# Optimization experiments

Hardware: AMD Instinct MI355X
Metric: run time of the kernel (lower is better)

The kernel has to match this reference:

```python
import jax, jax.numpy as jnp
import numpy as np
import math

N_GENES_TOTAL = 20000
N_CELLS_TOTAL = 10000
N_LATENT = 64
N_COMP = 32
SCALE_LOWER_BOUND = 1e-5
LOG_2PI = math.log(2.0 * math.pi)


def setup_inputs() -> dict:
    key = jax.random.key(0)
    ks = jax.random.split(key, 16)
    n_cells, n_genes = 512, 4000
    n_cuts, n_frags = 1000000, 1000000
    inp = {}
    inp["local_cellxgene_ix"] = jax.random.randint(ks[0], (n_frags,), 0, n_cells * n_genes)
    inp["cut_coordinates"] = jax.random.uniform(ks[1], (n_cuts,), dtype=jnp.float32)
    inp["latent"] = jax.random.normal(ks[2], (n_cells, N_LATENT), dtype=jnp.float32)
    inp["genes_oi"] = jax.random.randint(ks[3], (n_genes,), 0, N_GENES_TOTAL)
    inp["cells_oi"] = jax.random.randint(ks[4], (n_cells,), 0, N_CELLS_TOTAL)
    inp["cut_local_cellxgene_ix"] = jax.random.randint(ks[5], (n_cuts,), 0, n_cells * n_genes)
    inp["cut_local_gene_ix"] = jax.random.randint(ks[6], (n_cuts,), 0, n_genes)
    inp["n_cells"] = n_cells
    inp["n_genes"] = n_genes
    # Mixture parameters (per total gene)
    loc_init = jnp.linspace(0.0, 1.0, N_COMP + 2)[1:-1]  # (C,)
    inp["loc_w"] = jnp.broadcast_to(jax.scipy.special.logit(loc_init), (N_GENES_TOTAL, N_COMP)).astype(jnp.float32)
    inp["scale_w"] = jnp.full((N_GENES_TOTAL, N_COMP), math.log(1.0 / N_COMP / 5.0), dtype=jnp.float32)
    inp["logit_w"] = (jax.random.normal(ks[7], (N_GENES_TOTAL, N_COMP)) / math.sqrt(N_COMP)).astype(jnp.float32)
    # Decoder sparse embeddings (n_layers=0 -> input dim = n_latent)
    stdv_l = 1.0 / math.sqrt(N_LATENT)
    inp["logit_weight"] = jax.random.uniform(ks[8], (N_GENES_TOTAL, N_LATENT, N_COMP), minval=-stdv_l, maxval=stdv_l, dtype=jnp.float32)
    stdv_r = 1.0 / math.sqrt(N_LATENT) / 100.0
    inp["rho_weight"] = jax.random.uniform(ks[9], (N_GENES_TOTAL, N_LATENT), minval=-stdv_r, maxval=stdv_r, dtype=jnp.float32)
    inp["rho_bias"] = jax.random.uniform(ks[10], (N_GENES_TOTAL,), minval=1e-4, maxval=1e-2, dtype=jnp.float32)
    inp["libsize"] = jax.random.uniform(ks[11], (N_CELLS_TOTAL,), minval=1000.0, maxval=10000.0, dtype=jnp.float32)
    return inp


def reference(local_cellxgene_ix, cut_coordinates, latent, genes_oi, cells_oi,
              cut_local_cellxgene_ix, cut_local_gene_ix, n_cells, n_genes,
              loc_w, scale_w, logit_w, logit_weight, rho_weight, rho_bias, libsize):
    # Decoder (n_layers=0 => nn_output == latent)
    lw = logit_weight[genes_oi]                      # [G, L, C]
    rw = rho_weight[genes_oi]                        # [G, L]
    mixture_delta = jnp.einsum("nl,glc->ngc", latent, lw)   # [N, G, C]
    rho = latent @ rw.T                               # [N, G]

    # Gather per-cut mixture delta
    C = mixture_delta.shape[-1]
    delta = mixture_delta.reshape(-1, C)[cut_local_cellxgene_ix]  # [K, C]

    # Mixture log prob
    loc = jax.nn.sigmoid(loc_w[genes_oi])[cut_local_gene_ix]                 # [K, C]
    scale = SCALE_LOWER_BOUND + jnp.exp(scale_w[genes_oi])[cut_local_gene_ix]  # [K, C]
    logits = logit_w[genes_oi][cut_local_gene_ix] + delta                    # [K, C]
    z = (cut_coordinates[:, None] - loc) / scale
    comp_lp = -0.5 * z * z - jnp.log(scale) - 0.5 * LOG_2PI                  # Normal log_prob
    likelihood_mixture = jax.scipy.special.logsumexp(jax.nn.log_softmax(logits, axis=-1) + comp_lp, axis=-1)  # [K]

    # Fragment count Poisson likelihood
    fragmentexpression = rho_bias[genes_oi][None, :] * jnp.exp(rho) * libsize[cells_oi][:, None]  # [N, G]
    counts = jnp.zeros((n_cells * n_genes,), dtype=jnp.float32).at[local_cellxgene_ix].add(1.0).reshape(n_cells, n_genes)
    likelihood_fragmentcounts = counts * jnp.log(fragmentexpression) - fragmentexpression - jax.lax.lgamma(counts + 1.0)

    elbo = -(likelihood_mixture.sum() + likelihood_fragmentcounts.sum())
    return elbo
```

## Files before the change

### kernel.cpp

```cpp
#include <hip/hip_runtime.h>


#define TPB 256
#define CHUNK 4096
#define MAXG 4096
#define MAXN 1024
#define HALF_LOG_2PI 0.9189385332046727f

typedef short bf16x8 __attribute__((ext_vector_type(8)));
typedef float f32x4 __attribute__((ext_vector_type(4)));

static __device__ __forceinline__ unsigned short f2bf(float f) {
  unsigned u = __float_as_uint(f);
  u += 0x7fffu + ((u >> 16) & 1u);
  return (unsigned short)(u >> 16);
}

static __device__ __forceinline__ float block_reduce(float v) {
  #pragma unroll
  for (int off = 32; off > 0; off >>= 1) v += __shfl_down(v, off, 64);
  __shared__ float wsum[4];
  if ((threadIdx.x & 63) == 0) wsum[threadIdx.x >> 6] = v;
  __syncthreads();
  return (threadIdx.x == 0) ? (wsum[0] + wsum[1] + wsum[2] + wsum[3]) : 0.f;
}

__global__ __launch_bounds__(TPB) void prep_hist_kernel(
    const int* __restrict__ cxg, const int* __restrict__ lix,
    unsigned* __restrict__ cntC, unsigned* __restrict__ cntF,
    const int* __restrict__ genes_oi,
    const float* __restrict__ loc_w, const float* __restrict__ scale_w,
    const float* __restrict__ logit_w, const float* __restrict__ latent,
    float4* __restrict__ gp, unsigned short* __restrict__ latbf,
    int K, int F, unsigned G, unsigned N, int B, int NL) {
  if ((int)blockIdx.x >= B) {
    int idx = ((int)blockIdx.x - B) * TPB + threadIdx.x;
    int ngp = (int)G * 32;
    if (idx < ngp) {
      int g = idx >> 5, c = idx & 31;
      long long gene = genes_oi[g];
      float lv = loc_w[gene * 32 + c];
      float loc = 1.f / (1.f + __expf(-lv));
      float sc = 1e-5f + __expf(scale_w[gene * 32 + c]);
      gp[idx] = make_float4(loc, 1.f / sc, -__logf(sc) - HALF_LOG_2PI, logit_w[gene * 32 + c]);
    } else if (idx - ngp < NL) {
      latbf[idx - ngp] = f2bf(latent[idx - ngp]);
    }
    return;
  }
  __shared__ unsigned hC[MAXG];
  __shared__ unsigned hF[MAXN];
  for (int t = threadIdx.x; t < MAXG; t += TPB) hC[t] = 0;
  for (int t = threadIdx.x; t < MAXN; t += TPB) hF[t] = 0;
  __syncthreads();
  int i0 = blockIdx.x * CHUNK;
  for (int t = threadIdx.x; t < CHUNK; t += TPB) {
    int i = i0 + t;
    if (i < K) { unsigned ix = (unsigned)cxg[i]; atomicAdd(&hC[ix % G], 1u); }
    if (i < F) { unsigned v = (unsigned)lix[i]; atomicAdd(&hF[v / G], 1u); }
  }
  __syncthreads();
  size_t b = blockIdx.x;
  for (unsigned t = threadIdx.x; t < G; t += TPB) cntC[b * G + t] = hC[t];
  for (unsigned t = threadIdx.x; t < N; t += TPB) cntF[b * N + t] = hF[t];
}

__global__ __launch_bounds__(TPB) void colscan_v2(
    unsigned* __restrict__ cntC, unsigned* __restrict__ cntF,
    unsigned* __restrict__ totC, unsigned* __restrict__ totF,
    int B, unsigned G, unsigned N) {
  unsigned wid = blockIdx.x * 4 + (threadIdx.x >> 6);
  int lane = threadIdx.x & 63;
  if (wid >= G + N) return;
  unsigned* col;
  unsigned stride;
  unsigned* tot;
  if (wid < G) { col = cntC + wid; stride = G; tot = totC + wid; }
  else         { col = cntF + (wid - G); stride = N; tot = totF + (wid - G); }
  unsigned base = 0;
  for (int b0 = 0; b0 < B; b0 += 64) {
    int b = b0 + lane;
    unsigned v = (b < B) ? col[(size_t)b * stride] : 0u;
    unsigned inc = v;
    #pragma unroll
    for (int d = 1; d < 64; d <<= 1) {
      unsigned t2 = __shfl_up(inc, d, 64);
      if (lane >= d) inc += t2;
    }
    if (b < B) col[(size_t)b * stride] = inc - v + base;
    base += __shfl(inc, 63, 64);
  }
  if (lane == 0) *tot = base;
}

__global__ __launch_bounds__(TPB) void scan2_v2(
    const unsigned* __restrict__ totC, unsigned* __restrict__ baseC, int SC, unsigned K,
    const unsigned* __restrict__ totF, unsigned* __restrict__ baseF, int SF, unsigned F,
    unsigned* __restrict__ ticket) {
  int lane = threadIdx.x & 63;
  int wv = threadIdx.x >> 6;
  if (wv == 0) {
    unsigned base = 0;
    for (int i0 = 0; i0 < SC; i0 += 64) {
      int i = i0 + lane;
      unsigned v = (i < SC) ? totC[i] : 0u;
      unsigned inc = v;
      #pragma unroll
      for (int d = 1; d < 64; d <<= 1) {
        unsigned t = __shfl_up(inc, d, 64);
        if (lane >= d) inc += t;
      }
      if (i < SC) baseC[i] = inc - v + base;
      base += __shfl(inc, 63, 64);
    }
    if (lane == 0) baseC[SC] = K;
  } else if (wv == 1) {
    unsigned base = 0;
    for (int i0 = 0; i0 < SF; i0 += 64) {
      int i = i0 + lane;
      unsigned v = (i < SF) ? totF[i] : 0u;
      unsigned inc = v;
      #pragma unroll
      for (int d = 1; d < 64; d <<= 1) {
        unsigned t = __shfl_up(inc, d, 64);
        if (lane >= d) inc += t;
      }
      if (i < SF) baseF[i] = inc - v + base;
      base += __shfl(inc, 63, 64);
    }
    if (lane == 0) baseF[SF] = F;
  } else if (threadIdx.x == 128) {
    *ticket = 0u;
  }
}

__global__ __launch_bounds__(TPB) void sort_pass3(
    const int* __restrict__ cxg, const int* __restrict__ lix,
    const float* __restrict__ xc, const int* __restrict__ gix,
    const unsigned* __restrict__ cntC, const unsigned* __restrict__ cntF,
    const unsigned* __restrict__ baseC, const unsigned* __restrict__ baseF,
    float2* __restrict__ pl, unsigned* __restrict__ fpl,
    int K, int F, unsigned G, unsigned N) {
  __shared__ unsigned cC[MAXG];
  __shared__ unsigned cF[MAXN];
  for (int t = threadIdx.x; t < MAXG; t += TPB) cC[t] = 0;
  for (int t = threadIdx.x; t < MAXN; t += TPB) cF[t] = 0;
  __syncthreads();
  int i0 = blockIdx.x * CHUNK;
  size_t b = blockIdx.x;
  for (int t = threadIdx.x; t < CHUNK; t += TPB) {
    int i = i0 + t;
    if (i < K) {
      unsigned ix = (unsigned)cxg[i];
      unsigned g = ix % G, n = ix / G;
      unsigned r = atomicAdd(&cC[g], 1u);
      unsigned pos = baseC[g] + cntC[b * G + g] + r;
      pl[pos] = make_float2(xc[i], __uint_as_float((n << 16) | (unsigned)gix[i]));
    }
    if (i < F) {
      unsigned v = (unsigned)lix[i];
      unsigned n = v / G, g = v - n * G;
      unsigned r = atomicAdd(&cF[n], 1u);
      fpl[baseF[n] + cntF[b * N + n] + r] = (n << 16) | g;
    }
  }
}

__global__ __launch_bounds__(TPB) void cuts_v6(
    const float2* __restrict__ pl, const unsigned short* __restrict__ latbf,
    const int* __restrict__ genes_oi, const float* __restrict__ logit_weight,
    const float4* __restrict__ gp, const unsigned* __restrict__ baseC,
    float* __restrict__ partials, unsigned G) {
  const int g = blockIdx.x;
  const int lane = threadIdx.x & 63;
  const int wv = threadIdx.x >> 6;
  const int quad = lane >> 4;
  const int r16 = lane & 15;

  const float* Wb = logit_weight + (size_t)genes_oi[g] * 2048;
  bf16x8 B0a, B1a, B0b, B1b;
  #pragma unroll
  for (int j = 0; j < 8; j++) {
    int l0 = quad * 8 + j;
    B0a[j] = (short)f2bf(Wb[l0 * 32 + r16]);
    B1a[j] = (short)f2bf(Wb[(l0 + 32) * 32 + r16]);
    B0b[j] = (short)f2bf(Wb[l0 * 32 + r16 + 16]);
    B1b[j] = (short)f2bf(Wb[(l0 + 32) * 32 + r16 + 16]);
  }

  const unsigned start = baseC[g], end = baseC[g + 1];
  const unsigned ntiles = (end - start + 15) >> 4;
  float lm = 0.f;

  for (unsigned t = wv; t < ntiles; t += 4) {
    unsigned kk0 = start + t * 16;
    unsigned idx = kk0 + r16;
    float2 p = pl[idx < end ? idx : start];
    unsigned u = __float_as_uint(p.y);
    const unsigned short* lb = latbf + (size_t)(u >> 16) * 64;
    bf16x8 A0 = *(const bf16x8*)(lb + quad * 8);
    bf16x8 A1 = *(const bf16x8*)(lb + 32 + quad * 8);

    f32x4 acc0 = {0.f, 0.f, 0.f, 0.f};
    f32x4 acc1 = {0.f, 0.f, 0.f, 0.f};
    acc0 = __builtin_amdgcn_mfma_f32_16x16x32_bf16(A0, B0a, acc0, 0, 0, 0);
    acc0 = __builtin_amdgcn_mfma_f32_16x16x32_bf16(A1, B1a, acc0, 0, 0, 0);
    acc1 = __builtin_amdgcn_mfma_f32_16x16x32_bf16(A0, B0b, acc1, 0, 0, 0);
    acc1 = __builtin_amdgcn_mfma_f32_16x16x32_bf16(A1, B1b, acc1, 0, 0, 0);

    #pragma unroll
    for (int r = 0; r < 4; r++) {
      int cut = quad * 4 + r;
      float xr = __shfl(p.x, cut, 64);
      unsigned ur = (unsigned)__shfl((int)u, cut, 64);
      unsigned gi = ur & 0xffffu;
      float4 q0 = gp[(size_t)gi * 32 + r16];
      float4 q1 = gp[(size_t)gi * 32 + r16 + 16];
      float t0 = q0.w + acc0[r], t1 = q1.w + acc1[r];
      float z0 = (xr - q0.x) * q0.y, z1 = (xr - q1.x) * q1.y;
      float u0 = t0 + fmaf(-0.5f * z0, z0, q0.z);
      float u1 = t1 + fmaf(-0.5f * z1, z1, q1.z);
      float e1 = __expf(u0) + __expf(u1);
      float e2 = __expf(t0) + __expf(t1);
      #pragma unroll
      for (int d = 1; d < 16; d <<= 1) {
        e1 += __shfl_xor(e1, d, 64);
        e2 += __shfl_xor(e2, d, 64);
      }
      if (r16 == 0 && (kk0 + (unsigned)cut) < end) lm += __logf(e1) - __logf(e2);
    }
  }
  float bs = block_reduce(lm);
  if (threadIdx.x == 0) partials[blockIdx.x] = bs;
}

__global__ __launch_bounds__(TPB) void pois_v5(
    const unsigned* __restrict__ fpl, const unsigned* __restrict__ baseF,
    const float* __restrict__ latent, const int* __restrict__ genes_oi,
    const int* __restrict__ cells_oi,
    const float* __restrict__ rho_weight, const float* __restrict__ rho_bias,
    const float* __restrict__ libsize,
    float* __restrict__ p1, int n1,
    float* __restrict__ p2, unsigned* __restrict__ ticket,
    float* __restrict__ out, int N, int G) {
  int n0 = blockIdx.x * 2;
  const int PB = gridDim.x;
  __shared__ unsigned cnt[2 * MAXG];
  for (int t = threadIdx.x; t < 2 * MAXG; t += TPB) cnt[t] = 0;
  __shared__ __align__(16) float lat[128];
  for (int t = threadIdx.x; t < 128; t += TPB) {
    int j = t >> 6, l = t & 63;
    lat[t] = (n0 + j < N) ? latent[(size_t)(n0 + j) * 64 + l] : 0.f;
  }
  __syncthreads();
  int nhi = min(n0 + 2, N);
  unsigned s0 = baseF[n0], e0 = baseF[nhi];
  for (unsigned i = s0 + threadIdx.x; i < e0; i += TPB) {
    unsigned v = fpl[i];
    unsigned j = (v >> 16) - (unsigned)n0, g = v & 0xffffu;
    atomicAdd(&cnt[j * MAXG + g], 1u);
  }
  __syncthreads();
  float lib0 = (n0 < N) ? libsize[cells_oi[n0]] : 0.f;
  float lib1 = (n0 + 1 < N) ? libsize[cells_oi[n0 + 1]] : 0.f;
  float sum = 0.f;
  for (int g = threadIdx.x; g < G; g += TPB) {
    long long gene = genes_oi[g];
    const float4* rw = (const float4*)(rho_weight + gene * 64);
    float r0 = 0.f, r1 = 0.f;
    #pragma unroll
    for (int i = 0; i < 16; i++) {
      float4 wv = rw[i];
      float4 l0 = *(const float4*)(&lat[i * 4]);
      float4 l1 = *(const float4*)(&lat[64 + i * 4]);
      r0 = fmaf(wv.x, l0.x, r0); r0 = fmaf(wv.y, l0.y, r0);
      r0 = fmaf(wv.z, l0.z, r0); r0 = fmaf(wv.w, l0.w, r0);
      r1 = fmaf(wv.x, l1.x, r1); r1 = fmaf(wv.y, l1.y, r1);
      r1 = fmaf(wv.z, l1.z, r1); r1 = fmaf(wv.w, l1.w, r1);
    }
    float rb = rho_bias[gene];
    if (n0 < N) {
      float fe = rb * __expf(r0) * lib0;
      unsigned c = cnt[g];
      float term = -fe;
      if (c) {
        float lf = 0.f;
        for (unsigned q2 = 2; q2 <= c; q2++) lf += __logf((float)q2);
        term += (float)c * __logf(fe) - lf;
      }
      sum += term;
    }
    if (n0 + 1 < N) {
      float fe = rb * __expf(r1) * lib1;
      unsigned c = cnt[MAXG + g];
      float term = -fe;
      if (c) {
        float lf = 0.f;
        for (unsigned q2 = 2; q2 <= c; q2++) lf += __logf((float)q2);
        term += (float)c * __logf(fe) - lf;
      }
      sum += term;
    }
  }
  float bs = block_reduce(sum);
  __shared__ unsigned slast;
  if (threadIdx.x == 0) {
    p2[blockIdx.x] = bs;
    __threadfence();
    slast = atomicAdd(ticket, 1u);
  }
  __syncthreads();
  if (slast == (unsigned)(PB - 1)) {
    __threadfence();
    float s = 0.f;
    for (int i = threadIdx.x; i < n1; i += TPB) s += p1[i];
    for (int i = threadIdx.x; i < PB; i += TPB) s += p2[i];
    float tot = block_reduce(s);
    if (threadIdx.x == 0) out[0] = -tot;
  }
}

extern "C" void kernel_launch(void* const* d_in, const int* in_sizes, int n_in,
                              void* d_out, int out_size, void* d_ws, size_t ws_size,
                              hipStream_t stream) {
  const int*   lix          = (const int*)d_in[0];
  const float* xc           = (const float*)d_in[1];
  const float* latent       = (const float*)d_in[2];
  const int*   genes_oi     = (const int*)d_in[3];
  const int*   cells_oi     = (const int*)d_in[4];
  const int*   cxg          = (const int*)d_in[5];
  const int*   gix          = (const int*)d_in[6];
  const float* loc_w        = (const float*)d_in[9];
  const float* scale_w      = (const float*)d_in[10];
  const float* logit_w      = (const float*)d_in[11];
  const float* logit_weight = (const float*)d_in[12];
  const float* rho_weight   = (const float*)d_in[13];
  const float* rho_bias     = (const float*)d_in[14];
  const float* libsize      = (const float*)d_in[15];
  float* out = (float*)d_out;

  const int F = in_sizes[0];
  const int K = in_sizes[1];
  const int N = in_sizes[2] / 64;
  const int G = in_sizes[3];
  const int NL = N * 64;

  const int M = (K > F) ? K : F;
  const int B = (M + CHUNK - 1) / CHUNK;
  const int PB = (N + 1) / 2;
  const int GPB = (G * 32 + NL + TPB - 1) / TPB;

  size_t off = 0;
  auto alloc = [&](size_t bytes) {
    size_t o = off;
    off = (off + bytes + 255) & ~(size_t)255;
    return o;
  };
  size_t cntC_off  = alloc((size_t)B * G * 4);
  size_t cntF_off  = alloc((size_t)B * N * 4);
  size_t totC_off  = alloc((size_t)G * 4);
  size_t totF_off  = alloc((size_t)N * 4);
  size_t baseC_off = alloc((size_t)(G + 1) * 4);
  size_t baseF_off = alloc((size_t)(N + 1) * 4);
  size_t pl_off    = alloc((size_t)K * 8);
  size_t fpl_off   = alloc((size_t)F * 4);
  size_t gp_off    = alloc((size_t)G * 32 * 16);
  size_t lb_off    = alloc((size_t)NL * 2);
  size_t p1_off    = alloc((size_t)G * 4);
  size_t p2_off    = alloc((size_t)PB * 4);
  size_t tk_off    = alloc(4);
  (void)ws_size;

  char* ws = (char*)d_ws;
  unsigned* cntC  = (unsigned*)(ws + cntC_off);
  unsigned* cntF  = (unsigned*)(ws + cntF_off);
  unsigned* totC  = (unsigned*)(ws + totC_off);
  unsigned* totF  = (unsigned*)(ws + totF_off);
  unsigned* baseC = (unsigned*)(ws + baseC_off);
  unsigned* baseF = (unsigned*)(ws + baseF_off);
  float2*   pl    = (float2*)(ws + pl_off);
  unsigned* fpl   = (unsigned*)(ws + fpl_off);
  float4*   gp    = (float4*)(ws + gp_off);
  unsigned short* latbf = (unsigned short*)(ws + lb_off);
  float*    p1    = (float*)(ws + p1_off);
  float*    p2    = (float*)(ws + p2_off);
  unsigned* ticket = (unsigned*)(ws + tk_off);

  prep_hist_kernel<<<B + GPB, TPB, 0, stream>>>(
      cxg, lix, cntC, cntF, genes_oi, loc_w, scale_w, logit_w, latent,
      gp, latbf, K, F, (unsigned)G, (unsigned)N, B, NL);
  colscan_v2<<<(G + N + 3) / 4, TPB, 0, stream>>>(
      cntC, cntF, totC, totF, B, (unsigned)G, (unsigned)N);
  scan2_v2<<<1, TPB, 0, stream>>>(totC, baseC, G, (unsigned)K,
                                  totF, baseF, N, (unsigned)F, ticket);
  sort_pass3<<<B, TPB, 0, stream>>>(cxg, lix, xc, gix, cntC, cntF, baseC, baseF,
                                    pl, fpl, K, F, (unsigned)G, (unsigned)N);
  cuts_v6<<<G, TPB, 0, stream>>>(pl, latbf, genes_oi, logit_weight, gp, baseC, p1, (unsigned)G);
  pois_v5<<<PB, TPB, 0, stream>>>(fpl, baseF, latent, genes_oi, cells_oi,
                                  rho_weight, rho_bias, libsize,
                                  p1, G, p2, ticket, out, N, G);
}
```

Baseline: 447.8 us.

## Bucket fragments by gene, fuse cuts and Poisson kernels, merge scans

Fragments are now bucketed by gene instead of by cell, so the Poisson term is computed per group of 4 genes across all cells. The mixture/cuts work and the Poisson work become one heterogeneous kernel launch with a single last-block reduction. The second-level scan is folded into the column-scan kernel through a last-block ticket. Together these remove two kernel launches and let the cuts and Poisson blocks overlap on the device. The cost is a larger gene-indexed fragment histogram (G columns instead of N) and extra work on the per-column scan and histogram stages.

New measurement: 723.7 us. 1.62x slower.

```diff
diff --git a/kernel.cpp b/kernel.cpp
--- a/kernel.cpp
+++ b/kernel.cpp
@@ -5,6 +5,7 @@
 #define CHUNK 4096
 #define MAXG 4096
 #define MAXN 1024
+#define GPG 4
 #define HALF_LOG_2PI 0.9189385332046727f
 
 typedef short bf16x8 __attribute__((ext_vector_type(8)));
@@ -32,8 +33,10 @@
     const float* __restrict__ loc_w, const float* __restrict__ scale_w,
     const float* __restrict__ logit_w, const float* __restrict__ latent,
     float4* __restrict__ gp, unsigned short* __restrict__ latbf,
-    int K, int F, unsigned G, unsigned N, int B, int NL) {
+    unsigned* __restrict__ ticket2,
+    int K, int F, unsigned G, int B, int NL) {
   if ((int)blockIdx.x >= B) {
+    if ((int)blockIdx.x == B && threadIdx.x == 0) *ticket2 = 0u;
     int idx = ((int)blockIdx.x - B) * TPB + threadIdx.x;
     int ngp = (int)G * 32;
     if (idx < ngp) {
@@ -49,88 +52,92 @@
     return;
   }
   __shared__ unsigned hC[MAXG];
-  __shared__ unsigned hF[MAXN];
-  for (int t = threadIdx.x; t < MAXG; t += TPB) hC[t] = 0;
-  for (int t = threadIdx.x; t < MAXN; t += TPB) hF[t] = 0;
+  __shared__ unsigned hF[MAXG];
+  for (int t = threadIdx.x; t < MAXG; t += TPB) { hC[t] = 0; hF[t] = 0; }
   __syncthreads();
   int i0 = blockIdx.x * CHUNK;
   for (int t = threadIdx.x; t < CHUNK; t += TPB) {
     int i = i0 + t;
     if (i < K) { unsigned ix = (unsigned)cxg[i]; atomicAdd(&hC[ix % G], 1u); }
-    if (i < F) { unsigned v = (unsigned)lix[i]; atomicAdd(&hF[v / G], 1u); }
+    if (i < F) { unsigned v = (unsigned)lix[i]; atomicAdd(&hF[v % G], 1u); }
   }
   __syncthreads();
   size_t b = blockIdx.x;
-  for (unsigned t = threadIdx.x; t < G; t += TPB) cntC[b * G + t] = hC[t];
-  for (unsigned t = threadIdx.x; t < N; t += TPB) cntF[b * N + t] = hF[t];
-}
-
-__global__ __launch_bounds__(TPB) void colscan_v2(
+  for (unsigned t = threadIdx.x; t < G; t += TPB) {
+    cntC[b * G + t] = hC[t];
+    cntF[b * G + t] = hF[t];
+  }
+}
+
+__global__ __launch_bounds__(TPB) void colscan_v3(
     unsigned* __restrict__ cntC, unsigned* __restrict__ cntF,
     unsigned* __restrict__ totC, unsigned* __restrict__ totF,
-    int B, unsigned G, unsigned N) {
+    unsigned* __restrict__ baseC, unsigned* __restrict__ baseF,
+    int B, unsigned G, unsigned K, unsigned F,
+    unsigned* __restrict__ ticket2, unsigned* __restrict__ ticket4, int NBLK) {
   unsigned wid = blockIdx.x * 4 + (threadIdx.x >> 6);
   int lane = threadIdx.x & 63;
-  if (wid >= G + N) return;
-  unsigned* col;
-  unsigned stride;
-  unsigned* tot;
-  if (wid < G) { col = cntC + wid; stride = G; tot = totC + wid; }
-  else         { col = cntF + (wid - G); stride = N; tot = totF + (wid - G); }
-  unsigned base = 0;
-  for (int b0 = 0; b0 < B; b0 += 64) {
-    int b = b0 + lane;
-    unsigned v = (b < B) ? col[(size_t)b * stride] : 0u;
-    unsigned inc = v;
-    #pragma unroll
-    for (int d = 1; d < 64; d <<= 1) {
-      unsigned t2 = __shfl_up(inc, d, 64);
-      if (lane >= d) inc += t2;
-    }
-    if (b < B) col[(size_t)b * stride] = inc - v + base;
-    base += __shfl(inc, 63, 64);
-  }
-  if (lane == 0) *tot = base;
-}
-
-__global__ __launch_bounds__(TPB) void scan2_v2(
-    const unsigned* __restrict__ totC, unsigned* __restrict__ baseC, int SC, unsigned K,
-    const unsigned* __restrict__ totF, unsigned* __restrict__ baseF, int SF, unsigned F,
-    unsigned* __restrict__ ticket) {
-  int lane = threadIdx.x & 63;
-  int wv = threadIdx.x >> 6;
-  if (wv == 0) {
+  if (wid < 2 * G) {
+    unsigned* col = (wid < G) ? (cntC + wid) : (cntF + (wid - G));
+    unsigned* tot = (wid < G) ? (totC + wid) : (totF + (wid - G));
     unsigned base = 0;
-    for (int i0 = 0; i0 < SC; i0 += 64) {
-      int i = i0 + lane;
-      unsigned v = (i < SC) ? totC[i] : 0u;
+    for (int b0 = 0; b0 < B; b0 += 64) {
+      int b = b0 + lane;
+      unsigned v = (b < B) ? col[(size_t)b * G] : 0u;
       unsigned inc = v;
       #pragma unroll
       for (int d = 1; d < 64; d <<= 1) {
-        unsigned t = __shfl_up(inc, d, 64);
-        if (lane >= d) inc += t;
-      }
-      if (i < SC) baseC[i] = inc - v + base;
+        unsigned t2 = __shfl_up(inc, d, 64);
+        if (lane >= d) inc += t2;
+      }
+      if (b < B) col[(size_t)b * G] = inc - v + base;
       base += __shfl(inc, 63, 64);
     }
-    if (lane == 0) baseC[SC] = K;
-  } else if (wv == 1) {
-    unsigned base = 0;
-    for (int i0 = 0; i0 < SF; i0 += 64) {
-      int i = i0 + lane;
-      unsigned v = (i < SF) ? totF[i] : 0u;
-      unsigned inc = v;
-      #pragma unroll
-      for (int d = 1; d < 64; d <<= 1) {
-        unsigned t = __shfl_up(inc, d, 64);
-        if (lane >= d) inc += t;
-      }
-      if (i < SF) baseF[i] = inc - v + base;
-      base += __shfl(inc, 63, 64);
-    }
-    if (lane == 0) baseF[SF] = F;
-  } else if (threadIdx.x == 128) {
-    *ticket = 0u;
+    if (lane == 0) *tot = base;
+  }
+  __syncthreads();
+  __shared__ unsigned sl;
+  if (threadIdx.x == 0) {
+    __threadfence();
+    sl = atomicAdd(ticket2, 1u);
+  }
+  __syncthreads();
+  if (sl == (unsigned)(NBLK - 1)) {
+    __threadfence();
+    int wv = threadIdx.x >> 6;
+    if (wv == 0) {
+      unsigned base = 0;
+      for (int i0 = 0; i0 < (int)G; i0 += 64) {
+        int i = i0 + lane;
+        unsigned v = (i < (int)G) ? totC[i] : 0u;
+        unsigned inc = v;
+        #pragma unroll
+        for (int d = 1; d < 64; d <<= 1) {
+          unsigned t = __shfl_up(inc, d, 64);
+          if (lane >= d) inc += t;
+        }
+        if (i < (int)G) baseC[i] = inc - v + base;
+        base += __shfl(inc, 63, 64);
+      }
+      if (lane == 0) baseC[G] = K;
+    } else if (wv == 1) {
+      unsigned base = 0;
+      for (int i0 = 0; i0 < (int)G; i0 += 64) {
+        int i = i0 + lane;
+        unsigned v = (i < (int)G) ? totF[i] : 0u;
+        unsigned inc = v;
+        #pragma unroll
+        for (int d = 1; d < 64; d <<= 1) {
+          unsigned t = __shfl_up(inc, d, 64);
+          if (lane >= d) inc += t;
+        }
+        if (i < (int)G) baseF[i] = inc - v + base;
+        base += __shfl(inc, 63, 64);
+      }
+      if (lane == 0) baseF[G] = F;
+    } else if (threadIdx.x == 128) {
+      *ticket4 = 0u;
+    }
   }
 }
 
@@ -140,11 +147,10 @@
     const unsigned* __restrict__ cntC, const unsigned* __restrict__ cntF,
     const unsigned* __restrict__ baseC, const unsigned* __restrict__ baseF,
     float2* __restrict__ pl, unsigned* __restrict__ fpl,
-    int K, int F, unsigned G, unsigned N) {
+    int K, int F, unsigned G) {
   __shared__ unsigned cC[MAXG];
-  __shared__ unsigned cF[MAXN];
-  for (int t = threadIdx.x; t < MAXG; t += TPB) cC[t] = 0;
-  for (int t = threadIdx.x; t < MAXN; t += TPB) cF[t] = 0;
+  __shared__ unsigned cF[MAXG];
+  for (int t = threadIdx.x; t < MAXG; t += TPB) { cC[t] = 0; cF[t] = 0; }
   __syncthreads();
   int i0 = blockIdx.x * CHUNK;
   size_t b = blockIdx.x;
@@ -159,162 +165,151 @@
     }
     if (i < F) {
       unsigned v = (unsigned)lix[i];
-      unsigned n = v / G, g = v - n * G;
-      unsigned r = atomicAdd(&cF[n], 1u);
-      fpl[baseF[n] + cntF[b * N + n] + r] = (n << 16) | g;
-    }
-  }
-}
-
-__global__ __launch_bounds__(TPB) void cuts_v6(
-    const float2* __restrict__ pl, const unsigned short* __restrict__ latbf,
-    const int* __restrict__ genes_oi, const float* __restrict__ logit_weight,
-    const float4* __restrict__ gp, const unsigned* __restrict__ baseC,
-    float* __restrict__ partials, unsigned G) {
-  const int g = blockIdx.x;
-  const int lane = threadIdx.x & 63;
-  const int wv = threadIdx.x >> 6;
-  const int quad = lane >> 4;
-  const int r16 = lane & 15;
-
-  const float* Wb = logit_weight + (size_t)genes_oi[g] * 2048;
-  bf16x8 B0a, B1a, B0b, B1b;
-  #pragma unroll
-  for (int j = 0; j < 8; j++) {
-    int l0 = quad * 8 + j;
-    B0a[j] = (short)f2bf(Wb[l0 * 32 + r16]);
-    B1a[j] = (short)f2bf(Wb[(l0 + 32) * 32 + r16]);
-    B0b[j] = (short)f2bf(Wb[l0 * 32 + r16 + 16]);
-    B1b[j] = (short)f2bf(Wb[(l0 + 32) * 32 + r16 + 16]);
-  }
-
-  const unsigned start = baseC[g], end = baseC[g + 1];
-  const unsigned ntiles = (end - start + 15) >> 4;
-  float lm = 0.f;
-
-  for (unsigned t = wv; t < ntiles; t += 4) {
-    unsigned kk0 = start + t * 16;
-    unsigned idx = kk0 + r16;
-    float2 p = pl[idx < end ? idx : start];
-    unsigned u = __float_as_uint(p.y);
-    const unsigned short* lb = latbf + (size_t)(u >> 16) * 64;
-    bf16x8 A0 = *(const bf16x8*)(lb + quad * 8);
-    bf16x8 A1 = *(const bf16x8*)(lb + 32 + quad * 8);
-
-    f32x4 acc0 = {0.f, 0.f, 0.f, 0.f};
-    f32x4 acc1 = {0.f, 0.f, 0.f, 0.f};
-    acc0 = __builtin_amdgcn_mfma_f32_16x16x32_bf16(A0, B0a, acc0, 0, 0, 0);
-    acc0 = __builtin_amdgcn_mfma_f32_16x16x32_bf16(A1, B1a, acc0, 0, 0, 0);
-    acc1 = __builtin_amdgcn_mfma_f32_16x16x32_bf16(A0, B0b, acc1, 0, 0, 0);
-    acc1 = __builtin_amdgcn_mfma_f32_16x16x32_bf16(A1, B1b, acc1, 0, 0, 0);
-
-    #pragma unroll
-    for (int r = 0; r < 4; r++) {
-      int cut = quad * 4 + r;
-      float xr = __shfl(p.x, cut, 64);
-      unsigned ur = (unsigned)__shfl((int)u, cut, 64);
-      unsigned gi = ur & 0xffffu;
-      float4 q0 = gp[(size_t)gi * 32 + r16];
-      float4 q1 = gp[(size_t)gi * 32 + r16 + 16];
-      float t0 = q0.w + acc0[r], t1 = q1.w + acc1[r];
-      float z0 = (xr - q0.x) * q0.y, z1 = (xr - q1.x) * q1.y;
-      float u0 = t0 + fmaf(-0.5f * z0, z0, q0.z);
-      float u1 = t1 + fmaf(-0.5f * z1, z1, q1.z);
-      float e1 = __expf(u0) + __expf(u1);
-      float e2 = __expf(t0) + __expf(t1);
-      #pragma unroll
-      for (int d = 1; d < 16; d <<= 1) {
-        e1 += __shfl_xor(e1, d, 64);
-        e2 += __shfl_xor(e2, d, 64);
-      }
-      if (r16 == 0 && (kk0 + (unsigned)cut) < end) lm += __logf(e1) - __logf(e2);
-    }
-  }
-  float bs = block_reduce(lm);
-  if (threadIdx.x == 0) partials[blockIdx.x] = bs;
-}
-
-__global__ __launch_bounds__(TPB) void pois_v5(
-    const unsigned* __restrict__ fpl, const unsigned* __restrict__ baseF,
-    const float* __restrict__ latent, const int* __restrict__ genes_oi,
-    const int* __restrict__ cells_oi,
+      unsigned g = v % G, n = v / G;
+      unsigned r = atomicAdd(&cF[g], 1u);
+      fpl[baseF[g] + cntF[b * G + g] + r] = n;
+    }
+  }
+}
+
+__global__ __launch_bounds__(TPB) void main_kernel(
+    const float2* __restrict__ pl, const unsigned* __restrict__ fpl,
+    const unsigned short* __restrict__ latbf, const float* __restrict__ latent,
+    const int* __restrict__ genes_oi, const int* __restrict__ cells_oi,
+    const float* __restrict__ logit_weight, const float4* __restrict__ gp,
     const float* __restrict__ rho_weight, const float* __restrict__ rho_bias,
     const float* __restrict__ libsize,
-    float* __restrict__ p1, int n1,
-    float* __restrict__ p2, unsigned* __restrict__ ticket,
-    float* __restrict__ out, int N, int G) {
-  int n0 = blockIdx.x * 2;
-  const int PB = gridDim.x;
-  __shared__ unsigned cnt[2 * MAXG];
-  for (int t = threadIdx.x; t < 2 * MAXG; t += TPB) cnt[t] = 0;
-  __shared__ __align__(16) float lat[128];
-  for (int t = threadIdx.x; t < 128; t += TPB) {
-    int j = t >> 6, l = t & 63;
-    lat[t] = (n0 + j < N) ? latent[(size_t)(n0 + j) * 64 + l] : 0.f;
-  }
-  __syncthreads();
-  int nhi = min(n0 + 2, N);
-  unsigned s0 = baseF[n0], e0 = baseF[nhi];
-  for (unsigned i = s0 + threadIdx.x; i < e0; i += TPB) {
-    unsigned v = fpl[i];
-    unsigned j = (v >> 16) - (unsigned)n0, g = v & 0xffffu;
-    atomicAdd(&cnt[j * MAXG + g], 1u);
-  }
-  __syncthreads();
-  float lib0 = (n0 < N) ? libsize[cells_oi[n0]] : 0.f;
-  float lib1 = (n0 + 1 < N) ? libsize[cells_oi[n0 + 1]] : 0.f;
-  float sum = 0.f;
-  for (int g = threadIdx.x; g < G; g += TPB) {
-    long long gene = genes_oi[g];
-    const float4* rw = (const float4*)(rho_weight + gene * 64);
-    float r0 = 0.f, r1 = 0.f;
+    const unsigned* __restrict__ baseC, const unsigned* __restrict__ baseF,
+    float* __restrict__ part, unsigned* __restrict__ ticket4,
+    float* __restrict__ out, int N, unsigned G, int NB) {
+  __shared__ __align__(16) float rwS[GPG * 64];
+  __shared__ float rbS[GPG];
+  __shared__ unsigned cnt[GPG * MAXN];
+  const int bid = blockIdx.x;
+  float lm = 0.f;
+
+  if (bid < (int)G) {
+    const int g = bid;
+    const int lane = threadIdx.x & 63;
+    const int wv = threadIdx.x >> 6;
+    const int quad = lane >> 4;
+    const int r16 = lane & 15;
+
+    const float* Wb = logit_weight + (size_t)genes_oi[g] * 2048;
+    bf16x8 B0a, B1a, B0b, B1b;
     #pragma unroll
-    for (int i = 0; i < 16; i++) {
-      float4 wv = rw[i];
-      float4 l0 = *(const float4*)(&lat[i * 4]);
-      float4 l1 = *(const float4*)(&lat[64 + i * 4]);
-      r0 = fmaf(wv.x, l0.x, r0); r0 = fmaf(wv.y, l0.y, r0);
-      r0 = fmaf(wv.z, l0.z, r0); r0 = fmaf(wv.w, l0.w, r0);
-      r1 = fmaf(wv.x, l1.x, r1); r1 = fmaf(wv.y, l1.y, r1);
-      r1 = fmaf(wv.z, l1.z, r1); r1 = fmaf(wv.w, l1.w, r1);
-    }
-    float rb = rho_bias[gene];
-    if (n0 < N) {
-      float fe = rb * __expf(r0) * lib0;
-      unsigned c = cnt[g];
-      float term = -fe;
-      if (c) {
-        float lf = 0.f;
-        for (unsigned q2 = 2; q2 <= c; q2++) lf += __logf((float)q2);
-        term += (float)c * __logf(fe) - lf;
-      }
-      sum += term;
-    }
-    if (n0 + 1 < N) {
-      float fe = rb * __expf(r1) * lib1;
-      unsigned c = cnt[MAXG + g];
-      float term = -fe;
-      if (c) {
-        float lf = 0.f;
-        for (unsigned q2 = 2; q2 <= c; q2++) lf += __logf((float)q2);
-        term += (float)c * __logf(fe) - lf;
-      }
-      sum += term;
-    }
-  }
-  float bs = block_reduce(sum);
-  __shared__ unsigned slast;
+    for (int j = 0; j < 8; j++) {
+      int l0 = quad * 8 + j;
+      B0a[j] = (short)f2bf(Wb[l0 * 32 + r16]);
+      B1a[j] = (short)f2bf(Wb[(l0 + 32) * 32 + r16]);
+      B0b[j] = (short)f2bf(Wb[l0 * 32 + r16 + 16]);
+      B1b[j] = (short)f2bf(Wb[(l0 + 32) * 32 + r16 + 16]);
+    }
+
+    const unsigned start = baseC[g], end = baseC[g + 1];
+    const unsigned ntiles = (end - start + 15) >> 4;
+    for (unsigned t = wv; t < ntiles; t += 4) {
+      unsigned kk0 = start + t * 16;
+      unsigned idx = kk0 + r16;
+      float2 p = pl[idx < end ? idx : start];
+      unsigned u = __float_as_uint(p.y);
+      const unsigned short* lb = latbf + (size_t)(u >> 16) * 64;
+      bf16x8 A0 = *(const bf16x8*)(lb + quad * 8);
+      bf16x8 A1 = *(const bf16x8*)(lb + 32 + quad * 8);
+
+      f32x4 acc0 = {0.f, 0.f, 0.f, 0.f};
+      f32x4 acc1 = {0.f, 0.f, 0.f, 0.f};
+      acc0 = __builtin_amdgcn_mfma_f32_16x16x32_bf16(A0, B0a, acc0, 0, 0, 0);
+      acc0 = __builtin_amdgcn_mfma_f32_16x16x32_bf16(A1, B1a, acc0, 0, 0, 0);
+      acc1 = __builtin_amdgcn_mfma_f32_16x16x32_bf16(A0, B0b, acc1, 0, 0, 0);
+      acc1 = __builtin_amdgcn_mfma_f32_16x16x32_bf16(A1, B1b, acc1, 0, 0, 0);
+
+      #pragma unroll
+      for (int r = 0; r < 4; r++) {
+        int cut = quad * 4 + r;
+        float xr = __shfl(p.x, cut, 64);
+        unsigned ur = (unsigned)__shfl((int)u, cut, 64);
+        unsigned gi = ur & 0xffffu;
+        float4 q0 = gp[(size_t)gi * 32 + r16];
+        float4 q1 = gp[(size_t)gi * 32 + r16 + 16];
+        float t0 = q0.w + acc0[r], t1 = q1.w + acc1[r];
+        float z0 = (xr - q0.x) * q0.y, z1 = (xr - q1.x) * q1.y;
+        float u0 = t0 + fmaf(-0.5f * z0, z0, q0.z);
+        float u1 = t1 + fmaf(-0.5f * z1, z1, q1.z);
+        float e1 = __expf(u0) + __expf(u1);
+        float e2 = __expf(t0) + __expf(t1);
+        #pragma unroll
+        for (int d = 1; d < 16; d <<= 1) {
+          e1 += __shfl_xor(e1, d, 64);
+          e2 += __shfl_xor(e2, d, 64);
+        }
+        if (r16 == 0 && (kk0 + (unsigned)cut) < end) lm += __logf(e1) - __logf(e2);
+      }
+    }
+  } else {
+    const int g0 = (bid - (int)G) * GPG;
+    {
+      int t = threadIdx.x;
+      int j = t >> 6, l = t & 63;
+      rwS[t] = (g0 + j < (int)G) ? rho_weight[(size_t)genes_oi[g0 + j] * 64 + l] : 0.f;
+      if (t < GPG) rbS[t] = (g0 + t < (int)G) ? rho_bias[genes_oi[g0 + t]] : 0.f;
+    }
+    for (int t = threadIdx.x; t < GPG * MAXN; t += TPB) cnt[t] = 0;
+    __syncthreads();
+    #pragma unroll
+    for (int j = 0; j < GPG; j++) {
+      if (g0 + j < (int)G) {
+        unsigned s = baseF[g0 + j], e = baseF[g0 + j + 1];
+        for (unsigned i = s + threadIdx.x; i < e; i += TPB)
+          atomicAdd(&cnt[j * MAXN + fpl[i]], 1u);
+      }
+    }
+    __syncthreads();
+    for (int n = threadIdx.x; n < N; n += TPB) {
+      const float4* latr = (const float4*)(latent + (size_t)n * 64);
+      float rho[GPG] = {0.f, 0.f, 0.f, 0.f};
+      #pragma unroll
+      for (int i = 0; i < 16; i++) {
+        float4 lv = latr[i];
+        #pragma unroll
+        for (int j = 0; j < GPG; j++) {
+          float4 w = *(const float4*)(&rwS[j * 64 + i * 4]);
+          rho[j] = fmaf(lv.x, w.x, rho[j]);
+          rho[j] = fmaf(lv.y, w.y, rho[j]);
+          rho[j] = fmaf(lv.z, w.z, rho[j]);
+          rho[j] = fmaf(lv.w, w.w, rho[j]);
+        }
+      }
+      float lib = libsize[cells_oi[n]];
+      #pragma unroll
+      for (int j = 0; j < GPG; j++) {
+        if (g0 + j < (int)G) {
+          float fe = rbS[j] * __expf(rho[j]) * lib;
+          unsigned c = cnt[j * MAXN + n];
+          float term = -fe;
+          if (c) {
+            float lf = 0.f;
+            for (unsigned q2 = 2; q2 <= c; q2++) lf += __logf((float)q2);
+            term += (float)c * __logf(fe) - lf;
+          }
+          lm += term;
+        }
+      }
+    }
+  }
+
+  float bs = block_reduce(lm);
+  __shared__ unsigned sl;
   if (threadIdx.x == 0) {
-    p2[blockIdx.x] = bs;
+    part[bid] = bs;
     __threadfence();
-    slast = atomicAdd(ticket, 1u);
-  }
-  __syncthreads();
-  if (slast == (unsigned)(PB - 1)) {
+    sl = atomicAdd(ticket4, 1u);
+  }
+  __syncthreads();
+  if (sl == (unsigned)(NB - 1)) {
     __threadfence();
     float s = 0.f;
-    for (int i = threadIdx.x; i < n1; i += TPB) s += p1[i];
-    for (int i = threadIdx.x; i < PB; i += TPB) s += p2[i];
+    for (int i = threadIdx.x; i < NB; i += TPB) s += part[i];
     float tot = block_reduce(s);
     if (threadIdx.x == 0) out[0] = -tot;
   }
@@ -347,8 +342,10 @@
 
   const int M = (K > F) ? K : F;
   const int B = (M + CHUNK - 1) / CHUNK;
-  const int PB = (N + 1) / 2;
+  const int PGB = (G + GPG - 1) / GPG;
+  const int NB = G + PGB;
   const int GPB = (G * 32 + NL + TPB - 1) / TPB;
+  const int CSB = (2 * G + 3) / 4;
 
   size_t off = 0;
   auto alloc = [&](size_t bytes) {
@@ -357,18 +354,18 @@
     return o;
   };
   size_t cntC_off  = alloc((size_t)B * G * 4);
-  size_t cntF_off  = alloc((size_t)B * N * 4);
+  size_t cntF_off  = alloc((size_t)B * G * 4);
   size_t totC_off  = alloc((size_t)G * 4);
-  size_t totF_off  = alloc((size_t)N * 4);
+  size_t totF_off  = alloc((size_t)G * 4);
   size_t baseC_off = alloc((size_t)(G + 1) * 4);
-  size_t baseF_off = alloc((size_t)(N + 1) * 4);
+  size_t baseF_off = alloc((size_t)(G + 1) * 4);
   size_t pl_off    = alloc((size_t)K * 8);
   size_t fpl_off   = alloc((size_t)F * 4);
   size_t gp_off    = alloc((size_t)G * 32 * 16);
   size_t lb_off    = alloc((size_t)NL * 2);
-  size_t p1_off    = alloc((size_t)G * 4);
-  size_t p2_off    = alloc((size_t)PB * 4);
-  size_t tk_off    = alloc(4);
+  size_t part_off  = alloc((size_t)NB * 4);
+  size_t tk2_off   = alloc(4);
+  size_t tk4_off   = alloc(4);
   (void)ws_size;
 
   char* ws = (char*)d_ws;
@@ -382,21 +379,20 @@
   unsigned* fpl   = (unsigned*)(ws + fpl_off);
   float4*   gp    = (float4*)(ws + gp_off);
   unsigned short* latbf = (unsigned short*)(ws + lb_off);
-  float*    p1    = (float*)(ws + p1_off);
-  float*    p2    = (float*)(ws + p2_off);
-  unsigned* ticket = (unsigned*)(ws + tk_off);
+  float*    part  = (float*)(ws + part_off);
+  unsigned* ticket2 = (unsigned*)(ws + tk2_off);
+  unsigned* ticket4 = (unsigned*)(ws + tk4_off);
 
   prep_hist_kernel<<<B + GPB, TPB, 0, stream>>>(
       cxg, lix, cntC, cntF, genes_oi, loc_w, scale_w, logit_w, latent,
-      gp, latbf, K, F, (unsigned)G, (unsigned)N, B, NL);
-  colscan_v2<<<(G + N + 3) / 4, TPB, 0, stream>>>(
-      cntC, cntF, totC, totF, B, (unsigned)G, (unsigned)N);
-  scan2_v2<<<1, TPB, 0, stream>>>(totC, baseC, G, (unsigned)K,
-                                  totF, baseF, N, (unsigned)F, ticket);
+      gp, latbf, ticket2, K, F, (unsigned)G, B, NL);
+  colscan_v3<<<CSB, TPB, 0, stream>>>(
+      cntC, cntF, totC, totF, baseC, baseF, B, (unsigned)G,
+      (unsigned)K, (unsigned)F, ticket2, ticket4, CSB);
   sort_pass3<<<B, TPB, 0, stream>>>(cxg, lix, xc, gix, cntC, cntF, baseC, baseF,
-                                    pl, fpl, K, F, (unsigned)G, (unsigned)N);
-  cuts_v6<<<G, TPB, 0, stream>>>(pl, latbf, genes_oi, logit_weight, gp, baseC, p1, (unsigned)G);
-  pois_v5<<<PB, TPB, 0, stream>>>(fpl, baseF, latent, genes_oi, cells_oi,
-                                  rho_weight, rho_bias, libsize,
-                                  p1, G, p2, ticket, out, N, G);
-}
+                                    pl, fpl, K, F, (unsigned)G);
+  main_kernel<<<NB, TPB, 0, stream>>>(
+      pl, fpl, latbf, latent, genes_oi, cells_oi, logit_weight, gp,
+      rho_weight, rho_bias, libsize, baseC, baseF, part, ticket4, out,
+      N, (unsigned)G, NB);
+}
```
